# Kernel optimization log

Hardware: AMD Instinct MI355X
Metric: run time of the kernel (lower is better)

The kernel has to match this reference:

```python
import jax, jax.numpy as jnp
import numpy as np

N_NODES = 50000
N_EDGES = 800000
D = 128
N_REL = 237


def _layer(x, W_I, W_O, rel, b, src, dst):
    # messages over real edges: compose (sub) then project
    msg = (x[src] - rel[edge_safe(dst, None) if False else None] if False else (x[src] - rel_gather)) if False else None
    # (see clean version below)
    raise NotImplementedError


def compgcn_layer(x, W_I, W_O, rel, b, src, dst, etype):
    n = x.shape[0]
    # real edges: gather, compose (sub), project, scatter-add at dst
    msg = (x[src] - rel[etype]) @ W_I.T            # [E, out]
    aggr = jax.ops.segment_sum(msg, dst, num_segments=n)
    # self loops (added with edge_type 0): each node contributes to itself
    self_msg = (x - rel[0]) @ W_I.T                # [N, out]
    # update: aggregated messages + W_O(x) + bias
    return aggr + self_msg + x @ W_O.T + b


def setup_inputs() -> dict:
    key = jax.random.key(0)
    ks = jax.random.split(key, 12)
    x = jax.random.normal(ks[0], (N_NODES, D), dtype=jnp.float32)
    edge_index = jax.random.randint(ks[1], (2, N_EDGES), 0, N_NODES, dtype=jnp.int32)
    edge_type = jax.random.randint(ks[2], (N_EDGES,), 0, N_REL, dtype=jnp.int32)
    def xavier(k, shape):
        bound = float(np.sqrt(6.0 / (shape[0] + shape[1])))
        return jax.random.uniform(k, shape, jnp.float32, -bound, bound)
    return {
        "x": x,
        "edge_index": edge_index,
        "edge_type": edge_type,
        "W_I1": xavier(ks[3], (D, D)), "W_O1": xavier(ks[4], (D, D)),
        "rel1": xavier(ks[5], (N_REL, D)), "b1": jnp.zeros((D,), jnp.float32),
        "W_I2": xavier(ks[6], (D, D)), "W_O2": xavier(ks[7], (D, D)),
        "rel2": xavier(ks[8], (N_REL, D)), "b2": jnp.zeros((D,), jnp.float32),
    }


def reference(x, edge_index, edge_type, W_I1, W_O1, rel1, b1, W_I2, W_O2, rel2, b2):
    src, dst = edge_index[0], edge_index[1]
    h = compgcn_layer(x, W_I1, W_O1, rel1, b1, src, dst, edge_type)
    h = jax.nn.relu(h)  # dropout inactive in eval
    out = compgcn_layer(h, W_I2, W_O2, rel2, b2, src, dst, edge_type)
    return out
```

## Files before the change

### kernel.cpp

```cpp
#include <hip/hip_runtime.h>

#define D 128
#define CAP 3072

typedef __attribute__((ext_vector_type(8))) short short8;
typedef __attribute__((ext_vector_type(4))) float f32x4;

__device__ __forceinline__ float blo(unsigned w) { return __uint_as_float(w << 16); }
__device__ __forceinline__ float bhi(unsigned w) { return __uint_as_float(w & 0xFFFF0000u); }
__device__ __forceinline__ unsigned bpack(float a, float b) {
    unsigned ua = __float_as_uint(a), ub = __float_as_uint(b);
    ua += 0x7FFFu + ((ua >> 16) & 1u);
    ub += 0x7FFFu + ((ub >> 16) & 1u);
    return (ua >> 16) | (ub & 0xFFFF0000u);
}

__global__ __launch_bounds__(256) void setup_mega(
    const float* __restrict__ x,
    const int* __restrict__ srcA, const int* __restrict__ dstA,
    const int* __restrict__ etA,
    const float* __restrict__ WI1, const float* __restrict__ WO1,
    const float* __restrict__ WI2, const float* __restrict__ WO2,
    const float* __restrict__ rel1, const float* __restrict__ rel2,
    const float* __restrict__ b1, const float* __restrict__ b2,
    unsigned* __restrict__ A1,
    unsigned* __restrict__ Wt1, unsigned* __restrict__ Wt2,
    float* __restrict__ c1, float* __restrict__ c2,
    unsigned* __restrict__ rb1, unsigned* __restrict__ rb2,
    int* __restrict__ coarseCnt, unsigned* __restrict__ bulk,
    int N, int E, int relHalf, int nCoarse) {
    int tid = threadIdx.x;
    int bx = blockIdx.x;
    const int B1B = (E + 4095) / 4096;

    if (bx < B1B) {
        __shared__ unsigned pay[4096];
        __shared__ unsigned short ck[4096];
        __shared__ int hist[400];
        __shared__ int base[400];
        int e0 = bx * 4096;
        int cnt = E - e0; if (cnt > 4096) cnt = 4096;
        for (int i = tid; i < nCoarse; i += 256) hist[i] = 0;
        __syncthreads();
        for (int i = tid; i < cnt; i += 256) {
            int e = e0 + i;
            int d = dstA[e];
            pay[i] = (unsigned)srcA[e] | ((unsigned)etA[e] << 17) | ((unsigned)(d & 127) << 25);
            int c = d >> 7;
            ck[i] = (unsigned short)c;
            atomicAdd(&hist[c], 1);
        }
        __syncthreads();
        for (int i = tid; i < nCoarse; i += 256) {
            int h = hist[i];
            base[i] = (h > 0) ? (i * CAP + atomicAdd(&coarseCnt[i * 16], h)) : 0;
            hist[i] = 0;
        }
        __syncthreads();
        for (int i = tid; i < cnt; i += 256) {
            int c = ck[i];
            int pos = base[c] + atomicAdd(&hist[c], 1);
            bulk[pos] = pay[i];
        }
        return;
    }
    bx -= B1B;
    const int CB = (N * 32 + 255) / 256;
    if (bx < CB) {
        int idx = bx * 256 + tid;
        if (idx < N * 32) {
            int n = idx >> 5, q = idx & 31;
            float4 v = ((const float4*)x)[idx];
            uint2 o;
            o.x = bpack(v.x, v.y);
            o.y = bpack(v.z, v.w);
            *(uint2*)(A1 + (size_t)n * 128 + 64 + q * 2) = o;
        }
        return;
    }
    bx -= CB;
    if (bx < 128) {
        int layer = bx >> 6;
        const float* WI = layer ? WI2 : WI1;
        const float* WO = layer ? WO2 : WO1;
        unsigned* Wt = layer ? Wt2 : Wt1;
        int idx = (bx & 63) * 256 + tid;
        int j = idx >> 7;
        int kk = idx & 127;
        int k0 = kk * 2;
        float a, b;
        if (k0 < D) {
            a = WI[j * D + k0];
            b = WI[j * D + k0 + 1];
        } else {
            int kx = k0 - D;
            a = WI[j * D + kx]     + WO[j * D + kx];
            b = WI[j * D + kx + 1] + WO[j * D + kx + 1];
        }
        Wt[idx] = bpack(a, b);
        return;
    }
    bx -= 128;
    if (bx == 0) {
        int layer = tid >> 7;
        int j = tid & (D - 1);
        const float* WI = layer ? WI2 : WI1;
        const float* b  = layer ? b2  : b1;
        const float* rl = layer ? rel2 : rel1;
        float s = b[j];
        for (int k = 0; k < D; ++k) s = fmaf(-WI[j * D + k], rl[k], s);
        (layer ? c2 : c1)[j] = s;
        return;
    }
    bx -= 1;
    {
        int idx = bx * 256 + tid;
        if (idx < 2 * relHalf) {
            const float* src = (idx < relHalf) ? rel1 : rel2;
            unsigned* dst = (idx < relHalf) ? rb1 : rb2;
            int k = (idx < relHalf) ? idx : idx - relHalf;
            float4 v = ((const float4*)src)[k];
            uint2 o;
            o.x = bpack(v.x, v.y);
            o.y = bpack(v.z, v.w);
            *(uint2*)(dst + (size_t)k * 2) = o;
        }
    }
}

__global__ __launch_bounds__(512) void scan_coarse(const int* __restrict__ coarseCnt,
                                                   int* __restrict__ coarseBase,
                                                   int nCoarse, int E) {
    __shared__ int arr[512];
    int tid = threadIdx.x;
    int c = (tid < nCoarse) ? coarseCnt[tid * 16] : 0;
    arr[tid] = c;
    __syncthreads();
    for (int off = 1; off < 512; off <<= 1) {
        int v = (tid >= off) ? arr[tid - off] : 0;
        __syncthreads();
        arr[tid] += v;
        __syncthreads();
    }
    if (tid < nCoarse) coarseBase[tid] = arr[tid] - c;
    if (tid == nCoarse) coarseBase[tid] = E;
}

__global__ __launch_bounds__(256) void bucket2(const unsigned* __restrict__ bulk,
                                               const int* __restrict__ coarseCnt,
                                               const int* __restrict__ coarseBase,
                                               int* __restrict__ row_ptr,
                                               int* __restrict__ col,
                                               int N, int E, int nCoarse) {
    __shared__ unsigned pay[CAP];
    __shared__ int hist[128];
    __shared__ int cur[128];
    int c = blockIdx.x;
    int tid = threadIdx.x;
    int cnt = coarseCnt[c * 16];
    int cb  = coarseBase[c];
    const unsigned* seg = bulk + (size_t)c * CAP;
    if (tid < 128) hist[tid] = 0;
    __syncthreads();
    for (int i = tid; i < cnt; i += 256) {
        unsigned v = seg[i];
        pay[i] = v;
        atomicAdd(&hist[v >> 25], 1);
    }
    __syncthreads();
    int f = tid;
    int myCnt = (f < 128) ? hist[f] : 0;
    for (int off = 1; off < 128; off <<= 1) {
        int v = (f < 128 && f >= off) ? hist[f - off] : 0;
        __syncthreads();
        if (f < 128) hist[f] += v;
        __syncthreads();
    }
    if (f < 128) {
        int excl = hist[f] - myCnt;
        int d = (c << 7) + f;
        if (d < N) row_ptr[d] = cb + excl;
        cur[f] = cb + excl;
    }
    if (c == nCoarse - 1 && tid == 0) row_ptr[N] = E;
    __syncthreads();
    for (int i = tid; i < cnt; i += 256) {
        unsigned v = pay[i];
        int pos = atomicAdd(&cur[v >> 25], 1);
        col[pos] = (int)(v & 0x1FFFFFFu);
    }
}

__global__ __launch_bounds__(256) void gather_kernel(const unsigned* __restrict__ Asrc,
                                                     const int* __restrict__ col,
                                                     const int* __restrict__ row_ptr,
                                                     const unsigned* __restrict__ relb,
                                                     unsigned* __restrict__ Adst, int N) {
    int n = blockIdx.x * 4 + (threadIdx.x >> 6);
    if (n >= N) return;
    int lane = threadIdx.x & 63;
    int g = lane >> 4;
    int h = lane & 15;
    int beg = row_ptr[n];
    int end = row_ptr[n + 1];
    float s[8];
#pragma unroll
    for (int j = 0; j < 8; ++j) s[j] = 0.f;

    for (int base = beg; base < end; base += 64) {
        int ci = base + lane;
        unsigned cv = (unsigned)col[(ci < end) ? ci : beg];
        int m = end - base; if (m > 64) m = 64;
        int e = 0;
        for (; e + 16 <= m; e += 16) {
            uint4 u[4], r[4];
#pragma unroll
            for (int t = 0; t < 4; ++t) {
                unsigned c = (unsigned)__shfl((int)cv, e + 4 * t + g, 64);
                u[t] = ((const uint4*)(Asrc + (size_t)(c & 0x1FFFFu) * 128 + 64))[h];
                r[t] = ((const uint4*)(relb + (size_t)(c >> 17) * 64))[h];
            }
#pragma unroll
            for (int t = 0; t < 4; ++t) {
                s[0] += blo(u[t].x) - blo(r[t].x);
                s[1] += bhi(u[t].x) - bhi(r[t].x);
                s[2] += blo(u[t].y) - blo(r[t].y);
                s[3] += bhi(u[t].y) - bhi(r[t].y);
                s[4] += blo(u[t].z) - blo(r[t].z);
                s[5] += bhi(u[t].z) - bhi(r[t].z);
                s[6] += blo(u[t].w) - blo(r[t].w);
                s[7] += bhi(u[t].w) - bhi(r[t].w);
            }
        }
        for (; e + 4 <= m; e += 4) {
            unsigned c = (unsigned)__shfl((int)cv, e + g, 64);
            uint4 u = ((const uint4*)(Asrc + (size_t)(c & 0x1FFFFu) * 128 + 64))[h];
            uint4 r = ((const uint4*)(relb + (size_t)(c >> 17) * 64))[h];
            s[0] += blo(u.x) - blo(r.x);
            s[1] += bhi(u.x) - bhi(r.x);
            s[2] += blo(u.y) - blo(r.y);
            s[3] += bhi(u.y) - bhi(r.y);
            s[4] += blo(u.z) - blo(r.z);
            s[5] += bhi(u.z) - bhi(r.z);
            s[6] += blo(u.w) - blo(r.w);
            s[7] += bhi(u.w) - bhi(r.w);
        }
        if (e < m) {
            int idx = e + g;
            unsigned c = (unsigned)__shfl((int)cv, (idx < m) ? idx : 0, 64);
            if (idx < m) {
                uint4 u = ((const uint4*)(Asrc + (size_t)(c & 0x1FFFFu) * 128 + 64))[h];
                uint4 r = ((const uint4*)(relb + (size_t)(c >> 17) * 64))[h];
                s[0] += blo(u.x) - blo(r.x);
                s[1] += bhi(u.x) - bhi(r.x);
                s[2] += blo(u.y) - blo(r.y);
                s[3] += bhi(u.y) - bhi(r.y);
                s[4] += blo(u.z) - blo(r.z);
                s[5] += bhi(u.z) - bhi(r.z);
                s[6] += blo(u.w) - blo(r.w);
                s[7] += bhi(u.w) - bhi(r.w);
            }
        }
    }
#pragma unroll
    for (int j = 0; j < 8; ++j) {
        s[j] += __shfl_xor(s[j], 16, 64);
        s[j] += __shfl_xor(s[j], 32, 64);
    }
    if (g == 0) {
        uint4 o;
        o.x = bpack(s[0], s[1]);
        o.y = bpack(s[2], s[3]);
        o.z = bpack(s[4], s[5]);
        o.w = bpack(s[6], s[7]);
        ((uint4*)(Adst + (size_t)n * 128))[h] = o;
    }
}

__global__ __launch_bounds__(256) void node_mfma(
    const unsigned* A,
    const unsigned* __restrict__ Wt,
    const float* __restrict__ cvec,
    float* outf,
    unsigned* __restrict__ outb,
    int do_relu, int N) {
    __shared__ unsigned WtS[128 * 32];
    __shared__ unsigned AS[128 * 32];
    int tid = threadIdx.x;
    int w = tid >> 6;
    int lane = tid & 63;
    int m = lane & 15;
    int quad = lane >> 4;
    int nbase = blockIdx.x * 128;

    f32x4 acc[2][8];
#pragma unroll
    for (int nt = 0; nt < 2; ++nt)
#pragma unroll
        for (int t = 0; t < 8; ++t) acc[nt][t] = (f32x4)(0.f);

    for (int kc = 0; kc < 4; ++kc) {
        for (int i = tid; i < 1024; i += 256) {
            int j = i >> 3, q = i & 7;
            uint4 v = ((const uint4*)Wt)[j * 32 + kc * 8 + q];
            *(uint4*)&WtS[j * 32 + 4 * (q ^ (j & 7))] = v;
        }
        for (int i = tid; i < 1024; i += 256) {
            int n = i >> 3, q = i & 7;
            int gn = nbase + n;
            uint4 v = make_uint4(0u, 0u, 0u, 0u);
            if (gn < N) v = ((const uint4*)A)[(size_t)gn * 32 + kc * 8 + q];
            *(uint4*)&AS[n * 32 + 4 * (q ^ (n & 7))] = v;
        }
        __syncthreads();

#pragma unroll
        for (int s = 0; s < 2; ++s) {
            int g = s * 4 + quad;
            int r0 = w * 32 + m;
            int r1 = r0 + 16;
            short8 b0 = *(const short8*)&AS[r0 * 32 + 4 * (g ^ (r0 & 7))];
            short8 b1 = *(const short8*)&AS[r1 * 32 + 4 * (g ^ (r1 & 7))];
#pragma unroll
            for (int t = 0; t < 8; ++t) {
                int jr = t * 16 + m;
                short8 a = *(const short8*)&WtS[jr * 32 + 4 * (g ^ (jr & 7))];
                acc[0][t] = __builtin_amdgcn_mfma_f32_16x16x32_bf16(a, b0, acc[0][t], 0, 0, 0);
                acc[1][t] = __builtin_amdgcn_mfma_f32_16x16x32_bf16(a, b1, acc[1][t], 0, 0, 0);
            }
        }
        __syncthreads();
    }

#pragma unroll
    for (int nt = 0; nt < 2; ++nt) {
        int node = nbase + w * 32 + nt * 16 + m;
        if (node < N) {
#pragma unroll
            for (int t = 0; t < 8; ++t) {
                float4 cv = ((const float4*)cvec)[t * 4 + quad];
                f32x4 a = acc[nt][t];
                float v0 = a[0] + cv.x;
                float v1 = a[1] + cv.y;
                float v2 = a[2] + cv.z;
                float v3 = a[3] + cv.w;
                if (do_relu) {
                    v0 = fmaxf(v0, 0.f); v1 = fmaxf(v1, 0.f);
                    v2 = fmaxf(v2, 0.f); v3 = fmaxf(v3, 0.f);
                }
                if (outf) {
                    ((float4*)outf)[(size_t)node * 32 + t * 4 + quad] =
                        make_float4(v0, v1, v2, v3);
                } else {
                    uint2 o;
                    o.x = bpack(v0, v1);
                    o.y = bpack(v2, v3);
                    ((uint2*)(outb + (size_t)node * 128))[32 + t * 4 + quad] = o;
                }
            }
        }
    }
}

extern "C" void kernel_launch(void* const* d_in, const int* in_sizes, int n_in,
                              void* d_out, int out_size, void* d_ws, size_t ws_size,
                              hipStream_t stream) {
    const float* x    = (const float*)d_in[0];
    const int*   ei   = (const int*)d_in[1];
    const int*   et   = (const int*)d_in[2];
    const float* WI1  = (const float*)d_in[3];
    const float* WO1  = (const float*)d_in[4];
    const float* rel1 = (const float*)d_in[5];
    const float* b1   = (const float*)d_in[6];
    const float* WI2  = (const float*)d_in[7];
    const float* WO2  = (const float*)d_in[8];
    const float* rel2 = (const float*)d_in[9];
    const float* b2   = (const float*)d_in[10];

    const int E = in_sizes[2];
    const int N = in_sizes[0] / D;
    const int* src = ei;
    const int* dst = ei + E;
    const int nCoarse = (N + 127) / 128;

    unsigned* wsu  = (unsigned*)d_ws;
    unsigned* A1   = wsu;
    unsigned* Wt1  = A1 + (size_t)N * 128;
    unsigned* Wt2  = Wt1 + 16384;
    float*    cvec1 = (float*)(Wt2 + 16384);
    float*    cvec2 = cvec1 + D;
    unsigned* rb1  = (unsigned*)(cvec2 + D);
    unsigned* rb2  = rb1 + 237 * 64;
    int*      coarseCnt  = (int*)(rb2 + 237 * 64);
    int*      coarseBase = coarseCnt + 8192;
    int*      row_ptr    = coarseBase + 512;
    int*      col        = row_ptr + N + 4;
    unsigned* bulk       = (unsigned*)(col + E);

    unsigned* A2 = (unsigned*)d_out;

    const int relHalf = 237 * 32;
    const int B1B = (E + 4095) / 4096;
    const int CB = (N * 32 + 255) / 256;
    const int RB = (2 * relHalf + 255) / 256;

    hipMemsetAsync(coarseCnt, 0, 8192 * sizeof(int), stream);
    setup_mega<<<B1B + CB + 128 + 1 + RB, 256, 0, stream>>>(
        x, src, dst, et, WI1, WO1, WI2, WO2, rel1, rel2, b1, b2,
        A1, Wt1, Wt2, cvec1, cvec2, rb1, rb2,
        coarseCnt, bulk, N, E, relHalf, nCoarse);

    scan_coarse<<<1, 512, 0, stream>>>(coarseCnt, coarseBase, nCoarse, E);
    bucket2<<<nCoarse, 256, 0, stream>>>(bulk, coarseCnt, coarseBase,
                                         row_ptr, col, N, E, nCoarse);

    const int gather_blocks = (N + 3) / 4;
    const int node_blocks = (N + 127) / 128;

    gather_kernel<<<gather_blocks, 256, 0, stream>>>(A1, col, row_ptr, rb1, A1, N);
    node_mfma<<<node_blocks, 256, 0, stream>>>(A1, Wt1, cvec1,
                                               (float*)nullptr, A2, 1, N);

    gather_kernel<<<gather_blocks, 256, 0, stream>>>(A2, col, row_ptr, rb2, A2, N);
    node_mfma<<<node_blocks, 256, 0, stream>>>(A2, Wt2, cvec2,
                                               (float*)d_out, (unsigned*)nullptr, 0, N);
}
```

Baseline: 226.8 us.

## Fuse neighbor gather with MFMA projection and fold coarse scan into bucket kernel

Merges the per-node gather/aggregate kernel and the MFMA node projection into one kernel that aggregates 64 nodes into shared memory and then multiplies them directly. The self features are read straight from global memory instead of from a combined buffer. The separate coarse-scan kernel is removed; each bucket block now computes its own prefix by summing earlier counts. Features are stored in compact 64-word rows with separate X1/X2 buffers. The intent is to cut two launches per layer and the round trip of aggregates through global memory. The cost is that MFMA tiles shrink to 64 nodes, and each wave aggregates 16 nodes serially before any MFMA starts.

```diff
diff --git a/kernel.cpp b/kernel.cpp
--- a/kernel.cpp
+++ b/kernel.cpp
@@ -23,7 +23,7 @@
     const float* __restrict__ WI2, const float* __restrict__ WO2,
     const float* __restrict__ rel1, const float* __restrict__ rel2,
     const float* __restrict__ b1, const float* __restrict__ b2,
-    unsigned* __restrict__ A1,
+    unsigned* __restrict__ X1,
     unsigned* __restrict__ Wt1, unsigned* __restrict__ Wt2,
     float* __restrict__ c1, float* __restrict__ c2,
     unsigned* __restrict__ rb1, unsigned* __restrict__ rb2,
@@ -74,7 +74,7 @@
             uint2 o;
             o.x = bpack(v.x, v.y);
             o.y = bpack(v.z, v.w);
-            *(uint2*)(A1 + (size_t)n * 128 + 64 + q * 2) = o;
+            *(uint2*)(X1 + (size_t)n * 64 + q * 2) = o;
         }
         return;
     }
@@ -128,40 +128,29 @@
     }
 }
 
-__global__ __launch_bounds__(512) void scan_coarse(const int* __restrict__ coarseCnt,
-                                                   int* __restrict__ coarseBase,
-                                                   int nCoarse, int E) {
-    __shared__ int arr[512];
-    int tid = threadIdx.x;
-    int c = (tid < nCoarse) ? coarseCnt[tid * 16] : 0;
-    arr[tid] = c;
-    __syncthreads();
-    for (int off = 1; off < 512; off <<= 1) {
-        int v = (tid >= off) ? arr[tid - off] : 0;
-        __syncthreads();
-        arr[tid] += v;
-        __syncthreads();
-    }
-    if (tid < nCoarse) coarseBase[tid] = arr[tid] - c;
-    if (tid == nCoarse) coarseBase[tid] = E;
-}
-
 __global__ __launch_bounds__(256) void bucket2(const unsigned* __restrict__ bulk,
                                                const int* __restrict__ coarseCnt,
-                                               const int* __restrict__ coarseBase,
                                                int* __restrict__ row_ptr,
                                                int* __restrict__ col,
                                                int N, int E, int nCoarse) {
     __shared__ unsigned pay[CAP];
+    __shared__ int red[256];
     __shared__ int hist[128];
     __shared__ int cur[128];
     int c = blockIdx.x;
     int tid = threadIdx.x;
     int cnt = coarseCnt[c * 16];
-    int cb  = coarseBase[c];
     const unsigned* seg = bulk + (size_t)c * CAP;
     if (tid < 128) hist[tid] = 0;
+    int sum = 0;
+    for (int i = tid; i < c; i += 256) sum += coarseCnt[i * 16];
+    red[tid] = sum;
     __syncthreads();
+    for (int off = 128; off > 0; off >>= 1) {
+        if (tid < off) red[tid] += red[tid + off];
+        __syncthreads();
+    }
+    int cb = red[0];
     for (int i = tid; i < cnt; i += 256) {
         unsigned v = seg[i];
         pay[i] = v;
@@ -191,113 +180,116 @@
     }
 }
 
-__global__ __launch_bounds__(256) void gather_kernel(const unsigned* __restrict__ Asrc,
-                                                     const int* __restrict__ col,
-                                                     const int* __restrict__ row_ptr,
-                                                     const unsigned* __restrict__ relb,
-                                                     unsigned* __restrict__ Adst, int N) {
-    int n = blockIdx.x * 4 + (threadIdx.x >> 6);
-    if (n >= N) return;
-    int lane = threadIdx.x & 63;
-    int g = lane >> 4;
-    int h = lane & 15;
-    int beg = row_ptr[n];
-    int end = row_ptr[n + 1];
-    float s[8];
-#pragma unroll
-    for (int j = 0; j < 8; ++j) s[j] = 0.f;
-
-    for (int base = beg; base < end; base += 64) {
-        int ci = base + lane;
-        unsigned cv = (unsigned)col[(ci < end) ? ci : beg];
-        int m = end - base; if (m > 64) m = 64;
-        int e = 0;
-        for (; e + 16 <= m; e += 16) {
-            uint4 u[4], r[4];
-#pragma unroll
-            for (int t = 0; t < 4; ++t) {
-                unsigned c = (unsigned)__shfl((int)cv, e + 4 * t + g, 64);
-                u[t] = ((const uint4*)(Asrc + (size_t)(c & 0x1FFFFu) * 128 + 64))[h];
-                r[t] = ((const uint4*)(relb + (size_t)(c >> 17) * 64))[h];
-            }
-#pragma unroll
-            for (int t = 0; t < 4; ++t) {
-                s[0] += blo(u[t].x) - blo(r[t].x);
-                s[1] += bhi(u[t].x) - bhi(r[t].x);
-                s[2] += blo(u[t].y) - blo(r[t].y);
-                s[3] += bhi(u[t].y) - bhi(r[t].y);
-                s[4] += blo(u[t].z) - blo(r[t].z);
-                s[5] += bhi(u[t].z) - bhi(r[t].z);
-                s[6] += blo(u[t].w) - blo(r[t].w);
-                s[7] += bhi(u[t].w) - bhi(r[t].w);
-            }
-        }
-        for (; e + 4 <= m; e += 4) {
-            unsigned c = (unsigned)__shfl((int)cv, e + g, 64);
-            uint4 u = ((const uint4*)(Asrc + (size_t)(c & 0x1FFFFu) * 128 + 64))[h];
-            uint4 r = ((const uint4*)(relb + (size_t)(c >> 17) * 64))[h];
-            s[0] += blo(u.x) - blo(r.x);
-            s[1] += bhi(u.x) - bhi(r.x);
-            s[2] += blo(u.y) - blo(r.y);
-            s[3] += bhi(u.y) - bhi(r.y);
-            s[4] += blo(u.z) - blo(r.z);
-            s[5] += bhi(u.z) - bhi(r.z);
-            s[6] += blo(u.w) - blo(r.w);
-            s[7] += bhi(u.w) - bhi(r.w);
-        }
-        if (e < m) {
-            int idx = e + g;
-            unsigned c = (unsigned)__shfl((int)cv, (idx < m) ? idx : 0, 64);
-            if (idx < m) {
-                uint4 u = ((const uint4*)(Asrc + (size_t)(c & 0x1FFFFu) * 128 + 64))[h];
-                uint4 r = ((const uint4*)(relb + (size_t)(c >> 17) * 64))[h];
-                s[0] += blo(u.x) - blo(r.x);
-                s[1] += bhi(u.x) - bhi(r.x);
-                s[2] += blo(u.y) - blo(r.y);
-                s[3] += bhi(u.y) - bhi(r.y);
-                s[4] += blo(u.z) - blo(r.z);
-                s[5] += bhi(u.z) - bhi(r.z);
-                s[6] += blo(u.w) - blo(r.w);
-                s[7] += bhi(u.w) - bhi(r.w);
-            }
-        }
-    }
-#pragma unroll
-    for (int j = 0; j < 8; ++j) {
-        s[j] += __shfl_xor(s[j], 16, 64);
-        s[j] += __shfl_xor(s[j], 32, 64);
-    }
-    if (g == 0) {
-        uint4 o;
-        o.x = bpack(s[0], s[1]);
-        o.y = bpack(s[2], s[3]);
-        o.z = bpack(s[4], s[5]);
-        o.w = bpack(s[6], s[7]);
-        ((uint4*)(Adst + (size_t)n * 128))[h] = o;
-    }
-}
-
-__global__ __launch_bounds__(256) void node_mfma(
-    const unsigned* A,
+__global__ __launch_bounds__(256, 3) void fused_layer(
+    const unsigned* __restrict__ X,
+    const int* __restrict__ col,
+    const int* __restrict__ row_ptr,
+    const unsigned* __restrict__ relb,
     const unsigned* __restrict__ Wt,
     const float* __restrict__ cvec,
     float* outf,
     unsigned* __restrict__ outb,
     int do_relu, int N) {
+    __shared__ unsigned aggS[64 * 64];
     __shared__ unsigned WtS[128 * 32];
-    __shared__ unsigned AS[128 * 32];
     int tid = threadIdx.x;
     int w = tid >> 6;
     int lane = tid & 63;
+    int nbase = blockIdx.x * 64;
+
+    {
+        int g = lane >> 4;
+        int h = lane & 15;
+        for (int i = 0; i < 16; ++i) {
+            int n = nbase + w * 16 + i;
+            if (n >= N) break;
+            int beg = row_ptr[n];
+            int end = row_ptr[n + 1];
+            float s[8];
+#pragma unroll
+            for (int j = 0; j < 8; ++j) s[j] = 0.f;
+
+            for (int base = beg; base < end; base += 64) {
+                int ci = base + lane;
+                unsigned cv = (unsigned)col[(ci < end) ? ci : beg];
+                int mm = end - base; if (mm > 64) mm = 64;
+                int e = 0;
+                for (; e + 16 <= mm; e += 16) {
+                    uint4 u[4], r[4];
+#pragma unroll
+                    for (int t = 0; t < 4; ++t) {
+                        unsigned c = (unsigned)__shfl((int)cv, e + 4 * t + g, 64);
+                        u[t] = ((const uint4*)(X + (size_t)(c & 0x1FFFFu) * 64))[h];
+                        r[t] = ((const uint4*)(relb + (size_t)(c >> 17) * 64))[h];
+                    }
+#pragma unroll
+                    for (int t = 0; t < 4; ++t) {
+                        s[0] += blo(u[t].x) - blo(r[t].x);
+                        s[1] += bhi(u[t].x) - bhi(r[t].x);
+                        s[2] += blo(u[t].y) - blo(r[t].y);
+                        s[3] += bhi(u[t].y) - bhi(r[t].y);
+                        s[4] += blo(u[t].z) - blo(r[t].z);
+                        s[5] += bhi(u[t].z) - bhi(r[t].z);
+                        s[6] += blo(u[t].w) - blo(r[t].w);
+                        s[7] += bhi(u[t].w) - bhi(r[t].w);
+                    }
+                }
+                for (; e + 4 <= mm; e += 4) {
+                    unsigned c = (unsigned)__shfl((int)cv, e + g, 64);
+                    uint4 u = ((const uint4*)(X + (size_t)(c & 0x1FFFFu) * 64))[h];
+                    uint4 r = ((const uint4*)(relb + (size_t)(c >> 17) * 64))[h];
+                    s[0] += blo(u.x) - blo(r.x);
+                    s[1] += bhi(u.x) - bhi(r.x);
+                    s[2] += blo(u.y) - blo(r.y);
+                    s[3] += bhi(u.y) - bhi(r.y);
+                    s[4] += blo(u.z) - blo(r.z);
+                    s[5] += bhi(u.z) - bhi(r.z);
+                    s[6] += blo(u.w) - blo(r.w);
+                    s[7] += bhi(u.w) - bhi(r.w);
+                }
+                if (e < mm) {
+                    int idx = e + g;
+                    unsigned c = (unsigned)__shfl((int)cv, (idx < mm) ? idx : 0, 64);
+                    if (idx < mm) {
+                        uint4 u = ((const uint4*)(X + (size_t)(c & 0x1FFFFu) * 64))[h];
+                        uint4 r = ((const uint4*)(relb + (size_t)(c >> 17) * 64))[h];
+                        s[0] += blo(u.x) - blo(r.x);
+                        s[1] += bhi(u.x) - bhi(r.x);
+                        s[2] += blo(u.y) - blo(r.y);
+                        s[3] += bhi(u.y) - bhi(r.y);
+                        s[4] += blo(u.z) - blo(r.z);
+                        s[5] += bhi(u.z) - bhi(r.z);
+                        s[6] += blo(u.w) - blo(r.w);
+                        s[7] += bhi(u.w) - bhi(r.w);
+                    }
+                }
+            }
+#pragma unroll
+            for (int j = 0; j < 8; ++j) {
+                s[j] += __shfl_xor(s[j], 16, 64);
+                s[j] += __shfl_xor(s[j], 32, 64);
+            }
+            if (g == 0) {
+                uint4 o;
+                o.x = bpack(s[0], s[1]);
+                o.y = bpack(s[2], s[3]);
+                o.z = bpack(s[4], s[5]);
+                o.w = bpack(s[6], s[7]);
+                int lr = w * 16 + i;
+                *(uint4*)&aggS[lr * 64 + (h >> 3) * 32 + 4 * ((h & 7) ^ (lr & 7))] = o;
+            }
+        }
+    }
+    __syncthreads();
+
     int m = lane & 15;
     int quad = lane >> 4;
-    int nbase = blockIdx.x * 128;
-
-    f32x4 acc[2][8];
-#pragma unroll
-    for (int nt = 0; nt < 2; ++nt)
-#pragma unroll
-        for (int t = 0; t < 8; ++t) acc[nt][t] = (f32x4)(0.f);
+    f32x4 acc[8];
+#pragma unroll
+    for (int t = 0; t < 8; ++t) acc[t] = (f32x4)(0.f);
+
+    int r0 = w * 16 + m;
+    int gr0 = nbase + r0;
 
     for (int kc = 0; kc < 4; ++kc) {
         for (int i = tid; i < 1024; i += 256) {
@@ -305,58 +297,50 @@
             uint4 v = ((const uint4*)Wt)[j * 32 + kc * 8 + q];
             *(uint4*)&WtS[j * 32 + 4 * (q ^ (j & 7))] = v;
         }
-        for (int i = tid; i < 1024; i += 256) {
-            int n = i >> 3, q = i & 7;
-            int gn = nbase + n;
-            uint4 v = make_uint4(0u, 0u, 0u, 0u);
-            if (gn < N) v = ((const uint4*)A)[(size_t)gn * 32 + kc * 8 + q];
-            *(uint4*)&AS[n * 32 + 4 * (q ^ (n & 7))] = v;
-        }
         __syncthreads();
 
 #pragma unroll
         for (int s = 0; s < 2; ++s) {
-            int g = s * 4 + quad;
-            int r0 = w * 32 + m;
-            int r1 = r0 + 16;
-            short8 b0 = *(const short8*)&AS[r0 * 32 + 4 * (g ^ (r0 & 7))];
-            short8 b1 = *(const short8*)&AS[r1 * 32 + 4 * (g ^ (r1 & 7))];
+            int gq = s * 4 + quad;
+            short8 b0;
+            if (kc < 2) {
+                b0 = *(const short8*)&aggS[r0 * 64 + kc * 32 + 4 * (gq ^ (r0 & 7))];
+            } else {
+                uint4 xv = make_uint4(0u, 0u, 0u, 0u);
+                if (gr0 < N) xv = ((const uint4*)X)[(size_t)gr0 * 16 + (kc - 2) * 8 + gq];
+                b0 = *(const short8*)&xv;
+            }
 #pragma unroll
             for (int t = 0; t < 8; ++t) {
                 int jr = t * 16 + m;
-                short8 a = *(const short8*)&WtS[jr * 32 + 4 * (g ^ (jr & 7))];
-                acc[0][t] = __builtin_amdgcn_mfma_f32_16x16x32_bf16(a, b0, acc[0][t], 0, 0, 0);
-                acc[1][t] = __builtin_amdgcn_mfma_f32_16x16x32_bf16(a, b1, acc[1][t], 0, 0, 0);
-            }
-        }
-        __syncthreads();
-    }
-
-#pragma unroll
-    for (int nt = 0; nt < 2; ++nt) {
-        int node = nbase + w * 32 + nt * 16 + m;
-        if (node < N) {
-#pragma unroll
-            for (int t = 0; t < 8; ++t) {
-                float4 cv = ((const float4*)cvec)[t * 4 + quad];
-                f32x4 a = acc[nt][t];
-                float v0 = a[0] + cv.x;
-                float v1 = a[1] + cv.y;
-                float v2 = a[2] + cv.z;
-                float v3 = a[3] + cv.w;
-                if (do_relu) {
-                    v0 = fmaxf(v0, 0.f); v1 = fmaxf(v1, 0.f);
-                    v2 = fmaxf(v2, 0.f); v3 = fmaxf(v3, 0.f);
-                }
-                if (outf) {
-                    ((float4*)outf)[(size_t)node * 32 + t * 4 + quad] =
-                        make_float4(v0, v1, v2, v3);
-                } else {
-                    uint2 o;
-                    o.x = bpack(v0, v1);
-                    o.y = bpack(v2, v3);
-                    ((uint2*)(outb + (size_t)node * 128))[32 + t * 4 + quad] = o;
-                }
+                short8 a = *(const short8*)&WtS[jr * 32 + 4 * (gq ^ (jr & 7))];
+                acc[t] = __builtin_amdgcn_mfma_f32_16x16x32_bf16(a, b0, acc[t], 0, 0, 0);
+            }
+        }
+        __syncthreads();
+    }
+
+    if (gr0 < N) {
+#pragma unroll
+        for (int t = 0; t < 8; ++t) {
+            float4 cv = ((const float4*)cvec)[t * 4 + quad];
+            f32x4 a = acc[t];
+            float v0 = a[0] + cv.x;
+            float v1 = a[1] + cv.y;
+            float v2 = a[2] + cv.z;
+            float v3 = a[3] + cv.w;
+            if (do_relu) {
+                v0 = fmaxf(v0, 0.f); v1 = fmaxf(v1, 0.f);
+                v2 = fmaxf(v2, 0.f); v3 = fmaxf(v3, 0.f);
+            }
+            if (outf) {
+                ((float4*)outf)[(size_t)gr0 * 32 + t * 4 + quad] =
+                    make_float4(v0, v1, v2, v3);
+            } else {
+                uint2 o;
+                o.x = bpack(v0, v1);
+                o.y = bpack(v2, v3);
+                ((uint2*)(outb + (size_t)gr0 * 64))[t * 4 + quad] = o;
             }
         }
     }
@@ -384,20 +368,18 @@
     const int nCoarse = (N + 127) / 128;
 
     unsigned* wsu  = (unsigned*)d_ws;
-    unsigned* A1   = wsu;
-    unsigned* Wt1  = A1 + (size_t)N * 128;
+    unsigned* X1   = wsu;
+    unsigned* X2   = X1 + (size_t)N * 64;
+    unsigned* Wt1  = X2 + (size_t)N * 64;
     unsigned* Wt2  = Wt1 + 16384;
     float*    cvec1 = (float*)(Wt2 + 16384);
     float*    cvec2 = cvec1 + D;
     unsigned* rb1  = (unsigned*)(cvec2 + D);
     unsigned* rb2  = rb1 + 237 * 64;
     int*      coarseCnt  = (int*)(rb2 + 237 * 64);
-    int*      coarseBase = coarseCnt + 8192;
-    int*      row_ptr    = coarseBase + 512;
+    int*      row_ptr    = coarseCnt + 8192;
     int*      col        = row_ptr + N + 4;
     unsigned* bulk       = (unsigned*)(col + E);
-
-    unsigned* A2 = (unsigned*)d_out;
 
     const int relHalf = 237 * 32;
     const int B1B = (E + 4095) / 4096;
@@ -407,21 +389,19 @@
     hipMemsetAsync(coarseCnt, 0, 8192 * sizeof(int), stream);
     setup_mega<<<B1B + CB + 128 + 1 + RB, 256, 0, stream>>>(
         x, src, dst, et, WI1, WO1, WI2, WO2, rel1, rel2, b1, b2,
-        A1, Wt1, Wt2, cvec1, cvec2, rb1, rb2,
+        X1, Wt1, Wt2, cvec1, cvec2, rb1, rb2,
         coarseCnt, bulk, N, E, relHalf, nCoarse);
 
-    scan_coarse<<<1, 512, 0, stream>>>(coarseCnt, coarseBase, nCoarse, E);
-    bucket2<<<nCoarse, 256, 0, stream>>>(bulk, coarseCnt, coarseBase,
-                                         row_ptr, col, N, E, nCoarse);
-
-    const int gather_blocks = (N + 3) / 4;
-    const int node_blocks = (N + 127) / 128;
-
-    gather_kernel<<<gather_blocks, 256, 0, stream>>>(A1, col, row_ptr, rb1, A1, N);
-    node_mfma<<<node_blocks, 256, 0, stream>>>(A1, Wt1, cvec1,
-                                               (float*)nullptr, A2, 1, N);
-
-    gather_kernel<<<gather_blocks, 256, 0, stream>>>(A2, col, row_ptr, rb2, A2, N);
-    node_mfma<<<node_blocks, 256, 0, stream>>>(A2, Wt2, cvec2,
-                                               (float*)d_out, (unsigned*)nullptr, 0, N);
+    bucket2<<<nCoarse, 256, 0, stream>>>(bulk, coarseCnt, row_ptr, col,
+                                         N, E, nCoarse);
+
+    const int fused_blocks = (N + 63) / 64;
+
+    fused_layer<<<fused_blocks, 256, 0, stream>>>(
+        X1, col, row_ptr, rb1, Wt1, cvec1,
+        (float*)nullptr, X2, 1, N);
+
+    fused_layer<<<fused_blocks, 256, 0, stream>>>(
+        X2, col, row_ptr, rb2, Wt2, cvec2,
+        (float*)d_out, (unsigned*)nullptr, 0, N);
 }
```

Result: slower. 234.8 us (+3.5%).

## Fold coarse scan into bucket kernel and halve node tile in MFMA GEMM

Applied to the files above, without the earlier changes.

Removes the separate single-block scan_coarse launch: each bucket2 block now computes its own base offset by summing preceding coarse counts with a block reduction. Separately, node_mfma now processes 64 nodes per block instead of 128, doubling the grid and halving per-wave accumulators to raise occupancy and parallelism. The cost is redundant prefix-sum reads across blocks, and the weight tile is loaded into shared memory twice as often per node.

```diff
diff --git a/kernel.cpp b/kernel.cpp
--- a/kernel.cpp
+++ b/kernel.cpp
@@ -128,40 +128,29 @@
     }
 }
 
-__global__ __launch_bounds__(512) void scan_coarse(const int* __restrict__ coarseCnt,
-                                                   int* __restrict__ coarseBase,
-                                                   int nCoarse, int E) {
-    __shared__ int arr[512];
-    int tid = threadIdx.x;
-    int c = (tid < nCoarse) ? coarseCnt[tid * 16] : 0;
-    arr[tid] = c;
-    __syncthreads();
-    for (int off = 1; off < 512; off <<= 1) {
-        int v = (tid >= off) ? arr[tid - off] : 0;
-        __syncthreads();
-        arr[tid] += v;
-        __syncthreads();
-    }
-    if (tid < nCoarse) coarseBase[tid] = arr[tid] - c;
-    if (tid == nCoarse) coarseBase[tid] = E;
-}
-
 __global__ __launch_bounds__(256) void bucket2(const unsigned* __restrict__ bulk,
                                                const int* __restrict__ coarseCnt,
-                                               const int* __restrict__ coarseBase,
                                                int* __restrict__ row_ptr,
                                                int* __restrict__ col,
                                                int N, int E, int nCoarse) {
     __shared__ unsigned pay[CAP];
+    __shared__ int red[256];
     __shared__ int hist[128];
     __shared__ int cur[128];
     int c = blockIdx.x;
     int tid = threadIdx.x;
     int cnt = coarseCnt[c * 16];
-    int cb  = coarseBase[c];
     const unsigned* seg = bulk + (size_t)c * CAP;
     if (tid < 128) hist[tid] = 0;
+    int sum = 0;
+    for (int i = tid; i < c; i += 256) sum += coarseCnt[i * 16];
+    red[tid] = sum;
     __syncthreads();
+    for (int off = 128; off > 0; off >>= 1) {
+        if (tid < off) red[tid] += red[tid + off];
+        __syncthreads();
+    }
+    int cb = red[0];
     for (int i = tid; i < cnt; i += 256) {
         unsigned v = seg[i];
         pay[i] = v;
@@ -285,19 +274,17 @@
     unsigned* __restrict__ outb,
     int do_relu, int N) {
     __shared__ unsigned WtS[128 * 32];
-    __shared__ unsigned AS[128 * 32];
+    __shared__ unsigned AS[64 * 32];
     int tid = threadIdx.x;
     int w = tid >> 6;
     int lane = tid & 63;
     int m = lane & 15;
     int quad = lane >> 4;
-    int nbase = blockIdx.x * 128;
-
-    f32x4 acc[2][8];
-#pragma unroll
-    for (int nt = 0; nt < 2; ++nt)
-#pragma unroll
-        for (int t = 0; t < 8; ++t) acc[nt][t] = (f32x4)(0.f);
+    int nbase = blockIdx.x * 64;
+
+    f32x4 acc[8];
+#pragma unroll
+    for (int t = 0; t < 8; ++t) acc[t] = (f32x4)(0.f);
 
     for (int kc = 0; kc < 4; ++kc) {
         for (int i = tid; i < 1024; i += 256) {
@@ -305,7 +292,7 @@
             uint4 v = ((const uint4*)Wt)[j * 32 + kc * 8 + q];
             *(uint4*)&WtS[j * 32 + 4 * (q ^ (j & 7))] = v;
         }
-        for (int i = tid; i < 1024; i += 256) {
+        for (int i = tid; i < 512; i += 256) {
             int n = i >> 3, q = i & 7;
             int gn = nbase + n;
             uint4 v = make_uint4(0u, 0u, 0u, 0u);
@@ -317,46 +304,40 @@
 #pragma unroll
         for (int s = 0; s < 2; ++s) {
             int g = s * 4 + quad;
-            int r0 = w * 32 + m;
-            int r1 = r0 + 16;
+            int r0 = w * 16 + m;
             short8 b0 = *(const short8*)&AS[r0 * 32 + 4 * (g ^ (r0 & 7))];
-            short8 b1 = *(const short8*)&AS[r1 * 32 + 4 * (g ^ (r1 & 7))];
 #pragma unroll
             for (int t = 0; t < 8; ++t) {
                 int jr = t * 16 + m;
                 short8 a = *(const short8*)&WtS[jr * 32 + 4 * (g ^ (jr & 7))];
-                acc[0][t] = __builtin_amdgcn_mfma_f32_16x16x32_bf16(a, b0, acc[0][t], 0, 0, 0);
-                acc[1][t] = __builtin_amdgcn_mfma_f32_16x16x32_bf16(a, b1, acc[1][t], 0, 0, 0);
-            }
-        }
-        __syncthreads();
-    }
-
-#pragma unroll
-    for (int nt = 0; nt < 2; ++nt) {
-        int node = nbase + w * 32 + nt * 16 + m;
-        if (node < N) {
-#pragma unroll
-            for (int t = 0; t < 8; ++t) {
-                float4 cv = ((const float4*)cvec)[t * 4 + quad];
-                f32x4 a = acc[nt][t];
-                float v0 = a[0] + cv.x;
-                float v1 = a[1] + cv.y;
-                float v2 = a[2] + cv.z;
-                float v3 = a[3] + cv.w;
-                if (do_relu) {
-                    v0 = fmaxf(v0, 0.f); v1 = fmaxf(v1, 0.f);
-                    v2 = fmaxf(v2, 0.f); v3 = fmaxf(v3, 0.f);
-                }
-                if (outf) {
-                    ((float4*)outf)[(size_t)node * 32 + t * 4 + quad] =
-                        make_float4(v0, v1, v2, v3);
-                } else {
-                    uint2 o;
-                    o.x = bpack(v0, v1);
-                    o.y = bpack(v2, v3);
-                    ((uint2*)(outb + (size_t)node * 128))[32 + t * 4 + quad] = o;
-                }
+                acc[t] = __builtin_amdgcn_mfma_f32_16x16x32_bf16(a, b0, acc[t], 0, 0, 0);
+            }
+        }
+        __syncthreads();
+    }
+
+    int node = nbase + w * 16 + m;
+    if (node < N) {
+#pragma unroll
+        for (int t = 0; t < 8; ++t) {
+            float4 cv = ((const float4*)cvec)[t * 4 + quad];
+            f32x4 a = acc[t];
+            float v0 = a[0] + cv.x;
+            float v1 = a[1] + cv.y;
+            float v2 = a[2] + cv.z;
+            float v3 = a[3] + cv.w;
+            if (do_relu) {
+                v0 = fmaxf(v0, 0.f); v1 = fmaxf(v1, 0.f);
+                v2 = fmaxf(v2, 0.f); v3 = fmaxf(v3, 0.f);
+            }
+            if (outf) {
+                ((float4*)outf)[(size_t)node * 32 + t * 4 + quad] =
+                    make_float4(v0, v1, v2, v3);
+            } else {
+                uint2 o;
+                o.x = bpack(v0, v1);
+                o.y = bpack(v2, v3);
+                ((uint2*)(outb + (size_t)node * 128))[32 + t * 4 + quad] = o;
             }
         }
     }
@@ -392,8 +373,7 @@
     unsigned* rb1  = (unsigned*)(cvec2 + D);
     unsigned* rb2  = rb1 + 237 * 64;
     int*      coarseCnt  = (int*)(rb2 + 237 * 64);
-    int*      coarseBase = coarseCnt + 8192;
-    int*      row_ptr    = coarseBase + 512;
+    int*      row_ptr    = coarseCnt + 8192;
     int*      col        = row_ptr + N + 4;
     unsigned* bulk       = (unsigned*)(col + E);
 
@@ -410,12 +390,11 @@
         A1, Wt1, Wt2, cvec1, cvec2, rb1, rb2,
         coarseCnt, bulk, N, E, relHalf, nCoarse);
 
-    scan_coarse<<<1, 512, 0, stream>>>(coarseCnt, coarseBase, nCoarse, E);
-    bucket2<<<nCoarse, 256, 0, stream>>>(bulk, coarseCnt, coarseBase,
-                                         row_ptr, col, N, E, nCoarse);
+    bucket2<<<nCoarse, 256, 0, stream>>>(bulk, coarseCnt, row_ptr, col,
+                                         N, E, nCoarse);
 
     const int gather_blocks = (N + 3) / 4;
-    const int node_blocks = (N + 127) / 128;
+    const int node_blocks = (N + 63) / 64;
 
     gather_kernel<<<gather_blocks, 256, 0, stream>>>(A1, col, row_ptr, rb1, A1, N);
     node_mfma<<<node_blocks, 256, 0, stream>>>(A1, Wt1, cvec1,
```

Result: faster. 219.4 us, median of 2 (-3.3%).
